# Optimization experiments

Hardware: AMD Instinct MI355X
Metric: run time of the kernel (lower is better)

The kernel has to match this reference:

```python
import jax, jax.numpy as jnp
import numpy as np
import math

# model dims
B, S, T = 4, 256, 8
D_MODEL, D_STATE, N_HEAD, NUM_LAYERS = 256, 128, 4, 2
VOCAB = 32000
D_HEAD = D_STATE // N_HEAD
# AdaptiveLIFNeuron constants
TAU, BASE_THR, ADAPT, TARGET = 2.0, 1.0, 0.1, 0.02
DECAY = math.exp(-1.0 / TAU)


@jax.custom_vjp
def spike_fn(x):
    # spikingjelly surrogate.ATan forward = heaviside
    return (x >= 0).astype(x.dtype)

def _spike_fwd(x):
    return spike_fn(x), x

def _spike_bwd(x, g):
    # ATan surrogate gradient, alpha=2: 1 / (1 + (pi*x)^2)
    return (g / (1.0 + (math.pi * x) ** 2),)

spike_fn.defvjp(_spike_fwd, _spike_bwd)


def lif_step(x, v, thr):
    v_pot = v * DECAY + x
    spike = spike_fn(v_pot - jax.lax.stop_gradient(thr))
    v_new = v_pot * (1.0 - jax.lax.stop_gradient(spike))  # reset where spiked
    err = jax.lax.stop_gradient(spike.mean() - TARGET)    # torch.no_grad threshold update
    thr_new = jnp.maximum(thr + ADAPT * err, 0.5)
    return spike, v_new, thr_new


def ssm_layer(x_tbsd, A, C, Wq, bq, Wkv, bkv, Wo, bo):
    # x_tbsd: [T, B, S, d_model] spikes/embeddings, scanned over time
    scale = 1.0 / math.sqrt(D_HEAD)

    def step(carry, x_t):
        h, sv, ov, ts, to = carry
        st = h @ A.T                                      # [B,S,d_state]
        q = (h @ Wq.T + bq).reshape(B * S, N_HEAD, D_HEAD)
        kv = x_t @ Wkv.T + bkv                            # [B,S,2*d_state]
        k, v = jnp.split(kv, 2, axis=-1)
        k = k.reshape(B * S, N_HEAD, D_HEAD)
        v = v.reshape(B * S, N_HEAD, D_HEAD)
        # attention across all B*S positions (faithful to torch reshape)
        scores = jnp.einsum('ahd,bhd->hab', q, k) * scale  # [H, BS, BS]
        attn = jax.nn.softmax(scores, axis=-1)
        att = jnp.einsum('hab,bhd->ahd', attn, v).reshape(B, S, D_STATE)
        upd = st + att @ Wo.T + bo
        h2, sv2, ts2 = lif_step(upd, sv, ts)
        out_pot = h2 @ C.T                                 # [B,S,d_model]
        os_, ov2, to2 = lif_step(out_pot, ov, to)
        return (h2, sv2, ov2, ts2, to2), os_

    init = (jnp.zeros((B, S, D_STATE)), jnp.zeros((B, S, D_STATE)),
            jnp.zeros((B, S, D_MODEL)),
            jnp.full((D_STATE,), BASE_THR), jnp.full((D_MODEL,), BASE_THR))
    _, outs = jax.lax.scan(step, init, x_tbsd)
    return outs  # [T,B,S,d_model]


def setup_inputs() -> dict:
    key = jax.random.key(0)
    ks = jax.random.split(key, 8)
    nrm = lambda k, shape, s: jax.random.normal(k, shape, jnp.float32) * s
    L = NUM_LAYERS
    return {
        'input_ids': jax.random.randint(ks[0], (B, S), 0, VOCAB),
        'emb': nrm(ks[1], (VOCAB, D_MODEL), 0.02),
        'A': nrm(ks[2], (L, D_STATE, D_STATE), 1.0 / math.sqrt(D_STATE)),
        'C': nrm(ks[3], (L, D_MODEL, D_STATE), 1.0 / math.sqrt(D_STATE)),
        'Wq': nrm(ks[4], (L, D_STATE, D_STATE), 1.0 / math.sqrt(D_STATE)),
        'bq': jnp.zeros((L, D_STATE)),
        'Wkv': nrm(ks[5], (L, 2 * D_STATE, D_MODEL), 1.0 / math.sqrt(D_MODEL)),
        'bkv': jnp.zeros((L, 2 * D_STATE)),
        'Wo': nrm(ks[6], (L, D_STATE, D_STATE), 1.0 / math.sqrt(D_STATE)),
        'bo': jnp.zeros((L, D_STATE)),
        'Wout': nrm(ks[7], (VOCAB, D_MODEL), 1.0 / math.sqrt(D_MODEL)),
        'bout': jnp.zeros((VOCAB,)),
    }


def reference(input_ids, emb, A, C, Wq, bq, Wkv, bkv, Wo, bo, Wout, bout):
    tok = emb[input_ids]                                   # [B,S,d_model]
    # encoder_type='expand': replicate embedding over time steps
    hidden = jnp.broadcast_to(tok[None], (T, B, S, D_MODEL))
    for l in range(NUM_LAYERS):
        hidden = ssm_layer(hidden, A[l], C[l], Wq[l], bq[l],
                           Wkv[l], bkv[l], Wo[l], bo[l])
    time_integrated = hidden.mean(axis=0)                  # mean over time -> [B,S,d_model]
    logits = time_integrated @ Wout.T + bout               # output_projection -> [B,S,vocab]
    return logits
```

## Files before the change

kernel.cpp:

```cpp
#include <hip/hip_runtime.h>
#include <math.h>

#define BS_TOT   1024
#define DM       256
#define DST      128
#define TSTEPS   8
#define DECAYF   0.6065306597126334f
#define SCALEF   0.17677669529663689f
#define NE       (BS_TOT * DM)

__global__ void embed_k(const int* __restrict__ ids, const float* __restrict__ emb,
                        float* __restrict__ tok) {
    int r = blockIdx.x, c = threadIdx.x;
    tok[r * DM + c] = emb[(size_t)ids[r] * DM + c];
}

__global__ void init_k(float* __restrict__ hb0, float* __restrict__ hb1,
                       float* __restrict__ svb0, float* __restrict__ svb1,
                       float* __restrict__ ovb0, float* __restrict__ ovb1,
                       float* __restrict__ W1T, float* __restrict__ B1,
                       float* __restrict__ WoT, float* __restrict__ CT,
                       const float* __restrict__ Al, const float* __restrict__ Wql,
                       const float* __restrict__ bql, const float* __restrict__ Wol,
                       const float* __restrict__ Cl, int* __restrict__ cnts) {
    int i = blockIdx.x * 256 + threadIdx.x;
    if (i < BS_TOT * DST) { hb0[i] = 0.f; hb1[i] = 0.f; svb0[i] = 0.f; svb1[i] = 0.f; }
    ovb0[i] = 0.f; ovb1[i] = 0.f;
    if (i < 32768) {
        int k = i >> 8, n = i & 255;
        W1T[i] = (n < 128) ? Al[n * 128 + k] : Wql[(n - 128) * 128 + k];
        CT[i]  = Cl[n * 128 + k];
    }
    if (i < 16384) {
        int k = i >> 7, n = i & 127;
        WoT[i] = Wol[n * 128 + k];
    }
    if (i < 256) B1[i] = (i < 128) ? 0.f : bql[i - 128];
    if (i < 16) cnts[i] = 0;
}

__global__ __launch_bounds__(256) void ktrans_k(const float* __restrict__ kv,
                                                float* __restrict__ kT) {
    __shared__ float tile[64][133];
    const float* src = kv + (size_t)blockIdx.y * NE;
    float* dst = kT + (size_t)blockIdx.y * (128 * 1024);
    const int kc = blockIdx.x, tid = threadIdx.x;
#pragma unroll
    for (int i = 0; i < 32; ++i) {
        int idx = i * 256 + tid;
        int key = idx >> 7, d = idx & 127;
        tile[key][d] = src[(size_t)(kc * 64 + key) * 256 + d];
    }
    __syncthreads();
#pragma unroll
    for (int i = 0; i < 32; ++i) {
        int idx = i * 256 + tid;
        int d = idx >> 6, key = idx & 63;
        dst[(size_t)d * 1024 + kc * 64 + key] = tile[key][d];
    }
}

__global__ void mean_k(const float* __restrict__ outs, float* __restrict__ ti) {
    int i = blockIdx.x * 256 + threadIdx.x;
    float s = 0.f;
#pragma unroll
    for (int t = 0; t < TSTEPS; ++t) s += outs[t * NE + i];
    ti[i] = s * 0.125f;
}

template <int BM, int BN, int BK, int TM, int TN>
__global__ __launch_bounds__((BM / TM) * (BN / TN))
void gemm_k(const float* __restrict__ Amat, const float* __restrict__ Wmat,
            const float* __restrict__ bias, float* __restrict__ outp,
            int M, int N, int K) {
    constexpr int NT  = (BM / TM) * (BN / TN);
    constexpr int NXT = BN / TN;
    __shared__ float As[BK][BM + 4];
    __shared__ float Bs[BK][BN + 4];
    const int tid = threadIdx.x;
    const int n0 = blockIdx.x * BN, m0 = blockIdx.y * BM;
    const int tx = tid % NXT, ty = tid / NXT;
    float acc[TM][TN] = {};

    for (int k0 = 0; k0 < K; k0 += BK) {
#pragma unroll
        for (int i = 0; i < (BM * BK) / NT; ++i) {
            int idx = i * NT + tid;
            int kk = idx % BK, mm = idx / BK;
            As[kk][mm] = Amat[(size_t)(m0 + mm) * K + k0 + kk];
        }
#pragma unroll
        for (int i = 0; i < (BN * BK) / NT; ++i) {
            int idx = i * NT + tid;
            int kk = idx % BK, nn = idx / BK;
            Bs[kk][nn] = Wmat[(size_t)(n0 + nn) * K + k0 + kk];
        }
        __syncthreads();
#pragma unroll
        for (int kk = 0; kk < BK; ++kk) {
            float a[TM], b[TN];
#pragma unroll
            for (int i = 0; i < TM; ++i) a[i] = As[kk][ty * TM + i];
#pragma unroll
            for (int j = 0; j < TN; ++j) b[j] = Bs[kk][tx * TN + j];
#pragma unroll
            for (int i = 0; i < TM; ++i)
#pragma unroll
                for (int j = 0; j < TN; ++j) acc[i][j] += a[i] * b[j];
        }
        __syncthreads();
    }
#pragma unroll
    for (int i = 0; i < TM; ++i) {
        int mr = m0 + ty * TM + i;
#pragma unroll
        for (int j = 0; j < TN; ++j) {
            int nc = n0 + tx * TN + j;
            float x = acc[i][j];
            if (bias) x += bias[nc];
            outp[(size_t)mr * N + nc] = x;
        }
    }
}

__global__ __launch_bounds__(256) void fstep_k(
    const float* __restrict__ kT,
    const float* __restrict__ kv,
    const float* __restrict__ W1T,
    const float* __restrict__ B1,
    const float* __restrict__ WoT,
    const float* __restrict__ CT,
    const float* __restrict__ bo,
    const float* __restrict__ h_old,
    float* __restrict__ h_new,
    const float* __restrict__ sv_in, float* __restrict__ sv_out,
    const float* __restrict__ ov_in, float* __restrict__ ov_out,
    const float* __restrict__ att_in,
    float* __restrict__ att_out,
    float* __restrict__ outs_prev,
    int* __restrict__ cnt1, int* __restrict__ cnt2, int t, int do_B)
{
    __shared__ float p_s[1024 * 10];
    __shared__ float v_s[64 * 36];
    __shared__ float hA_s[8 * 128];
    __shared__ float h2_s[8 * 128];
    __shared__ float att_s[8 * 128];
    __shared__ float q_s[8 * 36];
    __shared__ float red_s[8 * 33];
    __shared__ float mrow_s[8], linv_s[8], thr_s[2];

    const int tid = threadIdx.x;
    const int hh = blockIdx.x >> 7;
    const int r0 = (blockIdx.x & 127) * 8;
    const bool wr = (hh == 0);

    if (t > 0) {
        if (tid == 0) {
            float ts = 1.0f, to = 1.0f;
            for (int i = 0; i < t - 1; ++i) {
                float e1 = (float)cnt1[i] * (1.f / 131072.f) - 0.02f;
                ts = fmaxf(ts + 0.1f * e1, 0.5f);
                float e2 = (float)cnt2[i] * (1.f / 262144.f) - 0.02f;
                to = fmaxf(to + 0.1f * e2, 0.5f);
            }
            thr_s[0] = ts; thr_s[1] = to;
        }
#pragma unroll
        for (int i = 0; i < 4; ++i) {
            int idx = i * 256 + tid;
            hA_s[idx]  = h_old[r0 * 128 + idx];
            att_s[idx] = att_in[r0 * 128 + idx];
        }
        __syncthreads();

        {
            const int n = tid & 127, half = tid >> 7;
            float st[4] = {0.f, 0.f, 0.f, 0.f};
            float b[4]  = {0.f, 0.f, 0.f, 0.f};
            for (int k4 = 0; k4 < 32; ++k4) {
                const int k = k4 * 4;
                float w10 = W1T[(k + 0) * 256 + n];
                float w11 = W1T[(k + 1) * 256 + n];
                float w12 = W1T[(k + 2) * 256 + n];
                float w13 = W1T[(k + 3) * 256 + n];
                float wo0 = WoT[(k + 0) * 128 + n];
                float wo1 = WoT[(k + 1) * 128 + n];
                float wo2 = WoT[(k + 2) * 128 + n];
                float wo3 = WoT[(k + 3) * 128 + n];
#pragma unroll
                for (int r4 = 0; r4 < 4; ++r4) {
                    int r = half * 4 + r4;
                    float4 hv = *(const float4*)&hA_s[r * 128 + k];
                    float4 av = *(const float4*)&att_s[r * 128 + k];
                    st[r4] += hv.x * w10; st[r4] += hv.y * w11;
                    st[r4] += hv.z * w12; st[r4] += hv.w * w13;
                    b[r4] += av.x * wo0; b[r4] += av.y * wo1;
                    b[r4] += av.z * wo2; b[r4] += av.w * wo3;
                }
            }
            float ts = thr_s[0];
            int my1 = 0;
#pragma unroll
            for (int r4 = 0; r4 < 4; ++r4) {
                int r = half * 4 + r4, row = r0 + r;
                float x = b[r4] + bo[n];
                x += st[r4];
                float v = sv_in[row * 128 + n];
                float vp = v * DECAYF + x;
                float sp = (vp - ts >= 0.f) ? 1.f : 0.f;
                h2_s[r * 128 + n] = sp;
                if (wr) {
                    h_new[row * 128 + n]  = sp;
                    sv_out[row * 128 + n] = vp * (1.f - sp);
                }
                my1 += (int)sp;
            }
            if (wr) {
#pragma unroll
                for (int off = 32; off > 0; off >>= 1) my1 += __shfl_down(my1, off, 64);
                if ((tid & 63) == 0) atomicAdd(&cnt1[t - 1], my1);
            }
        }
        __syncthreads();

        if (wr) {
            const int n = tid;
            float acc[8] = {0.f, 0.f, 0.f, 0.f, 0.f, 0.f, 0.f, 0.f};
            for (int k4 = 0; k4 < 32; ++k4) {
                const int k = k4 * 4;
                float c0 = CT[(k + 0) * 256 + n];
                float c1 = CT[(k + 1) * 256 + n];
                float c2 = CT[(k + 2) * 256 + n];
                float c3 = CT[(k + 3) * 256 + n];
#pragma unroll
                for (int r = 0; r < 8; ++r) {
                    float4 hv = *(const float4*)&h2_s[r * 128 + k];
                    acc[r] += hv.x * c0; acc[r] += hv.y * c1;
                    acc[r] += hv.z * c2; acc[r] += hv.w * c3;
                }
            }
            float to = thr_s[1];
            int my2 = 0;
#pragma unroll
            for (int r = 0; r < 8; ++r) {
                int row = r0 + r;
                float vo = ov_in[row * 256 + n];
                float vp = vo * DECAYF + acc[r];
                float sp = (vp - to >= 0.f) ? 1.f : 0.f;
                outs_prev[(size_t)row * 256 + n] = sp;
                ov_out[row * 256 + n] = vp * (1.f - sp);
                my2 += (int)sp;
            }
#pragma unroll
            for (int off = 32; off > 0; off >>= 1) my2 += __shfl_down(my2, off, 64);
            if ((tid & 63) == 0) atomicAdd(&cnt2[t - 1], my2);
        }
    } else {
#pragma unroll
        for (int i = 0; i < 4; ++i) {
            int idx = i * 256 + tid;
            h2_s[idx] = h_new[r0 * 128 + idx];
        }
        __syncthreads();
    }

    if (!do_B) return;

    {
        const int r = tid >> 5, d = tid & 31;
        const int col = 128 + hh * 32 + d;
        float acc = 0.f;
        for (int k4 = 0; k4 < 32; ++k4) {
            const int k = k4 * 4;
            float4 hv = *(const float4*)&h2_s[r * 128 + k];
            float w0 = W1T[(k + 0) * 256 + col];
            float w1 = W1T[(k + 1) * 256 + col];
            float w2 = W1T[(k + 2) * 256 + col];
            float w3 = W1T[(k + 3) * 256 + col];
            acc += hv.x * w0; acc += hv.y * w1; acc += hv.z * w2; acc += hv.w * w3;
        }
        q_s[r * 36 + d] = acc + B1[col];
    }
    __syncthreads();

    {
        const int w = tid >> 6, lane = tid & 63;
        float4 qr0[8], qr1[8];
#pragma unroll
        for (int d4 = 0; d4 < 8; ++d4) {
            qr0[d4] = *(const float4*)&q_s[(2 * w) * 36 + d4 * 4];
            qr1[d4] = *(const float4*)&q_s[(2 * w + 1) * 36 + d4 * 4];
        }
        const float* kTh = kT + hh * 32 * 1024;
        for (int kk = 0; kk < 16; ++kk) {
            const int key = kk * 64 + lane;
            float kreg[32];
#pragma unroll
            for (int d = 0; d < 32; ++d) kreg[d] = kTh[d * 1024 + key];
            float a0 = 0.f, a1 = 0.f;
#pragma unroll
            for (int d4 = 0; d4 < 8; ++d4) {
                a0 += qr0[d4].x * kreg[d4 * 4 + 0]; a0 += qr0[d4].y * kreg[d4 * 4 + 1];
                a0 += qr0[d4].z * kreg[d4 * 4 + 2]; a0 += qr0[d4].w * kreg[d4 * 4 + 3];
                a1 += qr1[d4].x * kreg[d4 * 4 + 0]; a1 += qr1[d4].y * kreg[d4 * 4 + 1];
                a1 += qr1[d4].z * kreg[d4 * 4 + 2]; a1 += qr1[d4].w * kreg[d4 * 4 + 3];
            }
            *(float2*)&p_s[key * 10 + 2 * w] = make_float2(a0 * SCALEF, a1 * SCALEF);
        }
    }
    __syncthreads();

    {
        const int rh = tid >> 5, lg = tid & 31;
        float mx = -1e30f;
        for (int jj = 0; jj < 32; ++jj)
            mx = fmaxf(mx, p_s[(lg + 32 * jj) * 10 + rh]);
        red_s[rh * 33 + lg] = mx;
        __syncthreads();
        if (tid < 8) {
            float m = red_s[tid * 33];
            for (int j = 1; j < 32; ++j) m = fmaxf(m, red_s[tid * 33 + j]);
            mrow_s[tid] = m;
        }
        __syncthreads();
        float m = mrow_s[rh];
        float ls = 0.f;
        for (int jj = 0; jj < 32; ++jj) {
            int a = (lg + 32 * jj) * 10 + rh;
            float p = expf(p_s[a] - m);
            p_s[a] = p;
            ls += p;
        }
        red_s[rh * 33 + lg] = ls;
        __syncthreads();
        if (tid < 8) {
            float l = 0.f;
            for (int j = 0; j < 32; ++j) l += red_s[tid * 33 + j];
            linv_s[tid] = 1.0f / l;
        }
    }
    __syncthreads();

    {
        const int pr = tid & 3;
        const int pd = (tid >> 2) & 15;
        const bool act = (tid < 64);
        const float4* kv4 = (const float4*)kv;
        float a00 = 0.f, a01 = 0.f, a10 = 0.f, a11 = 0.f;
        for (int c = 0; c < 16; ++c) {
            __syncthreads();
#pragma unroll
            for (int i = 0; i < 2; ++i) {
                int idx = i * 256 + tid;
                int key = idx >> 3, dq = idx & 7;
                *(float4*)&v_s[key * 36 + dq * 4] =
                    kv4[(size_t)(c * 64 + key) * 64 + 32 + hh * 8 + dq];
            }
            __syncthreads();
            if (act) {
#pragma unroll 8
                for (int j = 0; j < 64; ++j) {
                    int key = c * 64 + j;
                    float2 p2 = *(const float2*)&p_s[key * 10 + pr * 2];
                    float2 v2 = *(const float2*)&v_s[j * 36 + pd * 2];
                    a00 += p2.x * v2.x; a01 += p2.x * v2.y;
                    a10 += p2.y * v2.x; a11 += p2.y * v2.y;
                }
            }
        }
        if (act) {
            float li0 = linv_s[2 * pr], li1 = linv_s[2 * pr + 1];
            *(float2*)&att_out[(r0 + 2 * pr) * 128 + hh * 32 + 2 * pd] =
                make_float2(a00 * li0, a01 * li0);
            *(float2*)&att_out[(r0 + 2 * pr + 1) * 128 + hh * 32 + 2 * pd] =
                make_float2(a10 * li1, a11 * li1);
        }
    }
}

extern "C" void kernel_launch(void* const* d_in, const int* in_sizes, int n_in,
                              void* d_out, int out_size, void* d_ws, size_t ws_size,
                              hipStream_t stream) {
    (void)in_sizes; (void)n_in; (void)out_size; (void)ws_size;
    const int*   ids  = (const int*)d_in[0];
    const float* emb  = (const float*)d_in[1];
    const float* Aw   = (const float*)d_in[2];
    const float* Cw   = (const float*)d_in[3];
    const float* Wq   = (const float*)d_in[4];
    const float* bq   = (const float*)d_in[5];
    const float* Wkv  = (const float*)d_in[6];
    const float* bkv  = (const float*)d_in[7];
    const float* Wo   = (const float*)d_in[8];
    const float* bo   = (const float*)d_in[9];
    const float* Wout = (const float*)d_in[10];
    const float* bout = (const float*)d_in[11];
    float* out = (float*)d_out;
    float* ws  = (float*)d_ws;

    float* tok  = ws;
    float* bufA = tok  + NE;
    float* bufB = bufA + 8 * NE;
    float* kvb  = bufB + 8 * NE;
    float* kTb  = kvb  + 8 * NE;
    float* attb0 = kTb  + 8 * 131072;
    float* attb1 = attb0 + 131072;
    float* hb0  = attb1 + 131072;
    float* hb1  = hb0  + 131072;
    float* svb0 = hb1  + 131072;
    float* svb1 = svb0 + 131072;
    float* ovb0 = svb1 + 131072;
    float* ovb1 = ovb0 + 262144;
    float* ti   = ovb1 + 262144;
    float* W1T  = ti   + NE;
    float* B1   = W1T  + 32768;
    float* WoT  = B1   + 256;
    float* CT   = WoT  + 16384;
    int*   cnts = (int*)(CT + 32768);

    float* hb[2]   = {hb0, hb1};
    float* svb[2]  = {svb0, svb1};
    float* ovb[2]  = {ovb0, ovb1};
    float* attb[2] = {attb0, attb1};

    embed_k<<<dim3(1024), dim3(256), 0, stream>>>(ids, emb, tok);

    for (int l = 0; l < 2; ++l) {
        const float* Al   = Aw  + l * 16384;
        const float* Cl   = Cw  + l * 32768;
        const float* Wql  = Wq  + l * 16384;
        const float* bql  = bq  + l * 128;
        const float* Wkvl = Wkv + l * 65536;
        const float* bkvl = bkv + l * 256;
        const float* Wol  = Wo  + l * 16384;
        const float* bol  = bo  + l * 128;
        const float* xin  = (l == 0) ? tok : bufA;
        float* outs       = (l == 0) ? bufA : bufB;
        const int Mkv     = (l == 0) ? BS_TOT : 8 * BS_TOT;
        const int nt      = (l == 0) ? 1 : 8;

        init_k<<<dim3(1024), dim3(256), 0, stream>>>(hb0, hb1, svb0, svb1, ovb0, ovb1,
                                                     W1T, B1, WoT, CT,
                                                     Al, Wql, bql, Wol, Cl, cnts);

        gemm_k<64, 64, 16, 4, 4><<<dim3(256 / 64, Mkv / 64), dim3(256), 0, stream>>>(
            xin, Wkvl, bkvl, kvb, Mkv, 256, 256);

        ktrans_k<<<dim3(16, nt), dim3(256), 0, stream>>>(kvb, kTb);

        for (int t = 0; t <= TSTEPS; ++t) {
            const int do_B = (t < TSTEPS) ? 1 : 0;
            const int tt = (t < TSTEPS) ? t : (TSTEPS - 1);
            const float* kT_t = (l == 0) ? kTb : kTb + (size_t)tt * 131072;
            const float* kv_t = (l == 0) ? kvb : kvb + (size_t)tt * NE;
            float* outs_prev = outs + (size_t)((t > 0) ? (t - 1) : 0) * NE;
            const int grid = do_B ? 512 : 128;
            fstep_k<<<dim3(grid), dim3(256), 0, stream>>>(
                kT_t, kv_t, W1T, B1, WoT, CT, bol,
                hb[t & 1], hb[(t + 1) & 1],
                svb[t & 1], svb[(t + 1) & 1],
                ovb[t & 1], ovb[(t + 1) & 1],
                attb[(t + 1) & 1], attb[t & 1],
                outs_prev, cnts, cnts + 8, t, do_B);
        }
    }

    mean_k<<<dim3(1024), dim3(256), 0, stream>>>(bufB, ti);

    gemm_k<256, 32, 16, 8, 4><<<dim3(32000 / 32, BS_TOT / 256), dim3(256), 0, stream>>>(
        ti, Wout, bout, out, BS_TOT, 32000, 256);
}
```

Measured before the change: 1.288 ms.

## Read weights untransposed, restructure P·V with double-buffered V, retile output GEMM

Drops the per-layer weight transposes in init_k, and fstep_k now reads A, Wo, C and Wq rows directly as float4 (each thread strides along its own row rather than coalescing across n). The probability buffer is stored row-major per query and the P·V loop uses float4 probability reads with a register-staged double buffer for V tiles, removing one barrier per chunk. The final vocabulary GEMM switches to a 64x64 tile configuration. Per-thread row reads of weights may coalesce worse than the previous transposed layout.

```diff
diff --git a/kernel.cpp b/kernel.cpp
--- a/kernel.cpp
+++ b/kernel.cpp
@@ -18,24 +18,10 @@
 __global__ void init_k(float* __restrict__ hb0, float* __restrict__ hb1,
                        float* __restrict__ svb0, float* __restrict__ svb1,
                        float* __restrict__ ovb0, float* __restrict__ ovb1,
-                       float* __restrict__ W1T, float* __restrict__ B1,
-                       float* __restrict__ WoT, float* __restrict__ CT,
-                       const float* __restrict__ Al, const float* __restrict__ Wql,
-                       const float* __restrict__ bql, const float* __restrict__ Wol,
-                       const float* __restrict__ Cl, int* __restrict__ cnts) {
+                       int* __restrict__ cnts) {
     int i = blockIdx.x * 256 + threadIdx.x;
     if (i < BS_TOT * DST) { hb0[i] = 0.f; hb1[i] = 0.f; svb0[i] = 0.f; svb1[i] = 0.f; }
     ovb0[i] = 0.f; ovb1[i] = 0.f;
-    if (i < 32768) {
-        int k = i >> 8, n = i & 255;
-        W1T[i] = (n < 128) ? Al[n * 128 + k] : Wql[(n - 128) * 128 + k];
-        CT[i]  = Cl[n * 128 + k];
-    }
-    if (i < 16384) {
-        int k = i >> 7, n = i & 127;
-        WoT[i] = Wol[n * 128 + k];
-    }
-    if (i < 256) B1[i] = (i < 128) ? 0.f : bql[i - 128];
     if (i < 16) cnts[i] = 0;
 }
 
@@ -126,22 +112,21 @@
 __global__ __launch_bounds__(256) void fstep_k(
     const float* __restrict__ kT,
     const float* __restrict__ kv,
-    const float* __restrict__ W1T,
-    const float* __restrict__ B1,
-    const float* __restrict__ WoT,
-    const float* __restrict__ CT,
-    const float* __restrict__ bo,
-    const float* __restrict__ h_old,
-    float* __restrict__ h_new,
+    const float* __restrict__ A_w,
+    const float* __restrict__ Wq_w,
+    const float* __restrict__ bq_w,
+    const float* __restrict__ Wo_w,
+    const float* __restrict__ bo_w,
+    const float* __restrict__ C_w,
+    const float* __restrict__ h_old, float* __restrict__ h_new,
     const float* __restrict__ sv_in, float* __restrict__ sv_out,
     const float* __restrict__ ov_in, float* __restrict__ ov_out,
-    const float* __restrict__ att_in,
-    float* __restrict__ att_out,
+    const float* __restrict__ att_in, float* __restrict__ att_out,
     float* __restrict__ outs_prev,
     int* __restrict__ cnt1, int* __restrict__ cnt2, int t, int do_B)
 {
-    __shared__ float p_s[1024 * 10];
-    __shared__ float v_s[64 * 36];
+    __shared__ float p_s[8][1032];
+    __shared__ float v_s[2][64 * 36];
     __shared__ float hA_s[8 * 128];
     __shared__ float h2_s[8 * 128];
     __shared__ float att_s[8 * 128];
@@ -152,7 +137,7 @@
     const int tid = threadIdx.x;
     const int hh = blockIdx.x >> 7;
     const int r0 = (blockIdx.x & 127) * 8;
-    const bool wr = (hh == 0);
+    const bool wrb = (hh == 0);
 
     if (t > 0) {
         if (tid == 0) {
@@ -175,27 +160,23 @@
 
         {
             const int n = tid & 127, half = tid >> 7;
+            const float* Ar  = A_w  + n * 128;
+            const float* Wor = Wo_w + n * 128;
             float st[4] = {0.f, 0.f, 0.f, 0.f};
             float b[4]  = {0.f, 0.f, 0.f, 0.f};
             for (int k4 = 0; k4 < 32; ++k4) {
                 const int k = k4 * 4;
-                float w10 = W1T[(k + 0) * 256 + n];
-                float w11 = W1T[(k + 1) * 256 + n];
-                float w12 = W1T[(k + 2) * 256 + n];
-                float w13 = W1T[(k + 3) * 256 + n];
-                float wo0 = WoT[(k + 0) * 128 + n];
-                float wo1 = WoT[(k + 1) * 128 + n];
-                float wo2 = WoT[(k + 2) * 128 + n];
-                float wo3 = WoT[(k + 3) * 128 + n];
+                float4 wa = *(const float4*)(Ar + k);
+                float4 wo = *(const float4*)(Wor + k);
 #pragma unroll
                 for (int r4 = 0; r4 < 4; ++r4) {
                     int r = half * 4 + r4;
                     float4 hv = *(const float4*)&hA_s[r * 128 + k];
                     float4 av = *(const float4*)&att_s[r * 128 + k];
-                    st[r4] += hv.x * w10; st[r4] += hv.y * w11;
-                    st[r4] += hv.z * w12; st[r4] += hv.w * w13;
-                    b[r4] += av.x * wo0; b[r4] += av.y * wo1;
-                    b[r4] += av.z * wo2; b[r4] += av.w * wo3;
+                    st[r4] += hv.x * wa.x; st[r4] += hv.y * wa.y;
+                    st[r4] += hv.z * wa.z; st[r4] += hv.w * wa.w;
+                    b[r4] += av.x * wo.x; b[r4] += av.y * wo.y;
+                    b[r4] += av.z * wo.z; b[r4] += av.w * wo.w;
                 }
             }
             float ts = thr_s[0];
@@ -203,19 +184,19 @@
 #pragma unroll
             for (int r4 = 0; r4 < 4; ++r4) {
                 int r = half * 4 + r4, row = r0 + r;
-                float x = b[r4] + bo[n];
+                float x = b[r4] + bo_w[n];
                 x += st[r4];
                 float v = sv_in[row * 128 + n];
                 float vp = v * DECAYF + x;
                 float sp = (vp - ts >= 0.f) ? 1.f : 0.f;
                 h2_s[r * 128 + n] = sp;
-                if (wr) {
+                if (wrb) {
                     h_new[row * 128 + n]  = sp;
                     sv_out[row * 128 + n] = vp * (1.f - sp);
                 }
                 my1 += (int)sp;
             }
-            if (wr) {
+            if (wrb) {
 #pragma unroll
                 for (int off = 32; off > 0; off >>= 1) my1 += __shfl_down(my1, off, 64);
                 if ((tid & 63) == 0) atomicAdd(&cnt1[t - 1], my1);
@@ -223,20 +204,18 @@
         }
         __syncthreads();
 
-        if (wr) {
+        if (wrb) {
             const int n = tid;
+            const float* Cr = C_w + n * 128;
             float acc[8] = {0.f, 0.f, 0.f, 0.f, 0.f, 0.f, 0.f, 0.f};
             for (int k4 = 0; k4 < 32; ++k4) {
                 const int k = k4 * 4;
-                float c0 = CT[(k + 0) * 256 + n];
-                float c1 = CT[(k + 1) * 256 + n];
-                float c2 = CT[(k + 2) * 256 + n];
-                float c3 = CT[(k + 3) * 256 + n];
+                float4 wc = *(const float4*)(Cr + k);
 #pragma unroll
                 for (int r = 0; r < 8; ++r) {
                     float4 hv = *(const float4*)&h2_s[r * 128 + k];
-                    acc[r] += hv.x * c0; acc[r] += hv.y * c1;
-                    acc[r] += hv.z * c2; acc[r] += hv.w * c3;
+                    acc[r] += hv.x * wc.x; acc[r] += hv.y * wc.y;
+                    acc[r] += hv.z * wc.z; acc[r] += hv.w * wc.w;
                 }
             }
             float to = thr_s[1];
@@ -268,18 +247,17 @@
 
     {
         const int r = tid >> 5, d = tid & 31;
-        const int col = 128 + hh * 32 + d;
+        const int j = hh * 32 + d;
+        const float* Wqr = Wq_w + j * 128;
         float acc = 0.f;
         for (int k4 = 0; k4 < 32; ++k4) {
             const int k = k4 * 4;
+            float4 wv = *(const float4*)(Wqr + k);
             float4 hv = *(const float4*)&h2_s[r * 128 + k];
-            float w0 = W1T[(k + 0) * 256 + col];
-            float w1 = W1T[(k + 1) * 256 + col];
-            float w2 = W1T[(k + 2) * 256 + col];
-            float w3 = W1T[(k + 3) * 256 + col];
-            acc += hv.x * w0; acc += hv.y * w1; acc += hv.z * w2; acc += hv.w * w3;
-        }
-        q_s[r * 36 + d] = acc + B1[col];
+            acc += hv.x * wv.x; acc += hv.y * wv.y;
+            acc += hv.z * wv.z; acc += hv.w * wv.w;
+        }
+        q_s[r * 36 + d] = acc + bq_w[j];
     }
     __syncthreads();
 
@@ -305,7 +283,8 @@
                 a1 += qr1[d4].x * kreg[d4 * 4 + 0]; a1 += qr1[d4].y * kreg[d4 * 4 + 1];
                 a1 += qr1[d4].z * kreg[d4 * 4 + 2]; a1 += qr1[d4].w * kreg[d4 * 4 + 3];
             }
-            *(float2*)&p_s[key * 10 + 2 * w] = make_float2(a0 * SCALEF, a1 * SCALEF);
+            p_s[2 * w][key]     = a0 * SCALEF;
+            p_s[2 * w + 1][key] = a1 * SCALEF;
         }
     }
     __syncthreads();
@@ -313,8 +292,7 @@
     {
         const int rh = tid >> 5, lg = tid & 31;
         float mx = -1e30f;
-        for (int jj = 0; jj < 32; ++jj)
-            mx = fmaxf(mx, p_s[(lg + 32 * jj) * 10 + rh]);
+        for (int jj = 0; jj < 32; ++jj) mx = fmaxf(mx, p_s[rh][lg + 32 * jj]);
         red_s[rh * 33 + lg] = mx;
         __syncthreads();
         if (tid < 8) {
@@ -326,9 +304,9 @@
         float m = mrow_s[rh];
         float ls = 0.f;
         for (int jj = 0; jj < 32; ++jj) {
-            int a = (lg + 32 * jj) * 10 + rh;
-            float p = expf(p_s[a] - m);
-            p_s[a] = p;
+            int a = lg + 32 * jj;
+            float p = expf(p_s[rh][a] - m);
+            p_s[rh][a] = p;
             ls += p;
         }
         red_s[rh * 33 + lg] = ls;
@@ -342,37 +320,55 @@
     __syncthreads();
 
     {
-        const int pr = tid & 3;
-        const int pd = (tid >> 2) & 15;
-        const bool act = (tid < 64);
+        const int rp = (tid >> 4) & 3;
+        const int dp = tid & 15;
         const float4* kv4 = (const float4*)kv;
+        float4 stg0, stg1;
+        {
+            int i0 = tid, i1 = 256 + tid;
+            stg0 = kv4[(size_t)(i0 >> 3) * 64 + 32 + hh * 8 + (i0 & 7)];
+            stg1 = kv4[(size_t)(i1 >> 3) * 64 + 32 + hh * 8 + (i1 & 7)];
+        }
         float a00 = 0.f, a01 = 0.f, a10 = 0.f, a11 = 0.f;
         for (int c = 0; c < 16; ++c) {
+            float* vb = &v_s[c & 1][0];
+            {
+                int i0 = tid, i1 = 256 + tid;
+                *(float4*)&vb[(i0 >> 3) * 36 + (i0 & 7) * 4] = stg0;
+                *(float4*)&vb[(i1 >> 3) * 36 + (i1 & 7) * 4] = stg1;
+            }
+            if (c < 15) {
+                int i0 = tid, i1 = 256 + tid;
+                stg0 = kv4[(size_t)((c + 1) * 64 + (i0 >> 3)) * 64 + 32 + hh * 8 + (i0 & 7)];
+                stg1 = kv4[(size_t)((c + 1) * 64 + (i1 >> 3)) * 64 + 32 + hh * 8 + (i1 & 7)];
+            }
             __syncthreads();
-#pragma unroll
-            for (int i = 0; i < 2; ++i) {
-                int idx = i * 256 + tid;
-                int key = idx >> 3, dq = idx & 7;
-                *(float4*)&v_s[key * 36 + dq * 4] =
-                    kv4[(size_t)(c * 64 + key) * 64 + 32 + hh * 8 + dq];
-            }
-            __syncthreads();
-            if (act) {
-#pragma unroll 8
-                for (int j = 0; j < 64; ++j) {
-                    int key = c * 64 + j;
-                    float2 p2 = *(const float2*)&p_s[key * 10 + pr * 2];
-                    float2 v2 = *(const float2*)&v_s[j * 36 + pd * 2];
-                    a00 += p2.x * v2.x; a01 += p2.x * v2.y;
-                    a10 += p2.y * v2.x; a11 += p2.y * v2.y;
+            if (tid < 64) {
+#pragma unroll 4
+                for (int k4 = 0; k4 < 16; ++k4) {
+                    const int kb = k4 * 4;
+                    float4 p0 = *(const float4*)&p_s[2 * rp][c * 64 + kb];
+                    float4 p1 = *(const float4*)&p_s[2 * rp + 1][c * 64 + kb];
+                    float2 v0 = *(const float2*)&vb[(kb + 0) * 36 + 2 * dp];
+                    float2 v1 = *(const float2*)&vb[(kb + 1) * 36 + 2 * dp];
+                    float2 v2 = *(const float2*)&vb[(kb + 2) * 36 + 2 * dp];
+                    float2 v3 = *(const float2*)&vb[(kb + 3) * 36 + 2 * dp];
+                    a00 += p0.x * v0.x; a01 += p0.x * v0.y;
+                    a10 += p1.x * v0.x; a11 += p1.x * v0.y;
+                    a00 += p0.y * v1.x; a01 += p0.y * v1.y;
+                    a10 += p1.y * v1.x; a11 += p1.y * v1.y;
+                    a00 += p0.z * v2.x; a01 += p0.z * v2.y;
+                    a10 += p1.z * v2.x; a11 += p1.z * v2.y;
+                    a00 += p0.w * v3.x; a01 += p0.w * v3.y;
+                    a10 += p1.w * v3.x; a11 += p1.w * v3.y;
                 }
             }
         }
-        if (act) {
-            float li0 = linv_s[2 * pr], li1 = linv_s[2 * pr + 1];
-            *(float2*)&att_out[(r0 + 2 * pr) * 128 + hh * 32 + 2 * pd] =
+        if (tid < 64) {
+            float li0 = linv_s[2 * rp], li1 = linv_s[2 * rp + 1];
+            *(float2*)&att_out[(size_t)(r0 + 2 * rp) * 128 + hh * 32 + 2 * dp] =
                 make_float2(a00 * li0, a01 * li0);
-            *(float2*)&att_out[(r0 + 2 * pr + 1) * 128 + hh * 32 + 2 * pd] =
+            *(float2*)&att_out[(size_t)(r0 + 2 * rp + 1) * 128 + hh * 32 + 2 * dp] =
                 make_float2(a10 * li1, a11 * li1);
         }
     }
@@ -411,11 +407,7 @@
     float* ovb0 = svb1 + 131072;
     float* ovb1 = ovb0 + 262144;
     float* ti   = ovb1 + 262144;
-    float* W1T  = ti   + NE;
-    float* B1   = W1T  + 32768;
-    float* WoT  = B1   + 256;
-    float* CT   = WoT  + 16384;
-    int*   cnts = (int*)(CT + 32768);
+    int*   cnts = (int*)(ti + NE);
 
     float* hb[2]   = {hb0, hb1};
     float* svb[2]  = {svb0, svb1};
@@ -438,9 +430,8 @@
         const int Mkv     = (l == 0) ? BS_TOT : 8 * BS_TOT;
         const int nt      = (l == 0) ? 1 : 8;
 
-        init_k<<<dim3(1024), dim3(256), 0, stream>>>(hb0, hb1, svb0, svb1, ovb0, ovb1,
-                                                     W1T, B1, WoT, CT,
-                                                     Al, Wql, bql, Wol, Cl, cnts);
+        init_k<<<dim3(1024), dim3(256), 0, stream>>>(hb0, hb1, svb0, svb1,
+                                                     ovb0, ovb1, cnts);
 
         gemm_k<64, 64, 16, 4, 4><<<dim3(256 / 64, Mkv / 64), dim3(256), 0, stream>>>(
             xin, Wkvl, bkvl, kvb, Mkv, 256, 256);
@@ -455,7 +446,7 @@
             float* outs_prev = outs + (size_t)((t > 0) ? (t - 1) : 0) * NE;
             const int grid = do_B ? 512 : 128;
             fstep_k<<<dim3(grid), dim3(256), 0, stream>>>(
-                kT_t, kv_t, W1T, B1, WoT, CT, bol,
+                kT_t, kv_t, Al, Wql, bql, Wol, bol, Cl,
                 hb[t & 1], hb[(t + 1) & 1],
                 svb[t & 1], svb[(t + 1) & 1],
                 ovb[t & 1], ovb[(t + 1) & 1],
@@ -466,6 +457,6 @@
 
     mean_k<<<dim3(1024), dim3(256), 0, stream>>>(bufB, ti);
 
-    gemm_k<256, 32, 16, 8, 4><<<dim3(32000 / 32, BS_TOT / 256), dim3(256), 0, stream>>>(
+    gemm_k<64, 64, 16, 4, 4><<<dim3(32000 / 64, BS_TOT / 64), dim3(256), 0, stream>>>(
         ti, Wout, bout, out, BS_TOT, 32000, 256);
 }
```

Measured after the change: 1.351 ms. +4.9%, slower.
